# Performance work log

Measured on AMD Instinct MI355X. Metric: run time of the kernel, lower is better.

## Reference

```python
import jax, jax.numpy as jnp
import numpy as np

N_NODES = 50000
N_EDGES = 600000
N_GRAPHS = 64
D_FEAT = 128
DIM_H = 128
N_HOPS = 3
OUT_DIM = 10


def setup_inputs() -> dict:
    key = jax.random.key(0)
    ks = jax.random.split(key, 16)
    x = jax.random.normal(ks[0], (N_NODES, D_FEAT), dtype=jnp.float32)
    edge_index = jax.random.randint(ks[1], (2, N_EDGES), 0, N_NODES, dtype=jnp.int64)
    batch = jnp.sort(jax.random.randint(ks[2], (N_NODES,), 0, N_GRAPHS, dtype=jnp.int64))
    def glorot(k, shape):
        fan = shape[0] + shape[1]
        return jax.random.uniform(k, shape, jnp.float32, -1.0, 1.0) * np.sqrt(6.0 / fan)
    # GCNConv weights stored as [in, out]; Linear weights stored as [in, out]
    W1 = glorot(ks[3], (D_FEAT, DIM_H)); b1 = jnp.zeros((DIM_H,), jnp.float32)
    W2 = glorot(ks[4], (DIM_H, DIM_H)); b2 = jnp.zeros((DIM_H,), jnp.float32)
    W3 = glorot(ks[5], (DIM_H, DIM_H)); b3 = jnp.zeros((DIM_H,), jnp.float32)
    H3 = DIM_H * N_HOPS
    lin1_W = glorot(ks[6], (H3, H3)); lin1_b = jnp.zeros((H3,), jnp.float32)
    lin2_W = glorot(ks[7], (H3, OUT_DIM)); lin2_b = jnp.zeros((OUT_DIM,), jnp.float32)
    return {"x": x, "W1": W1, "b1": b1, "W2": W2, "b2": b2, "W3": W3, "b3": b3,
            "lin1_W": lin1_W, "lin1_b": lin1_b, "lin2_W": lin2_W, "lin2_b": lin2_b,
            "edge_index": edge_index, "batch": batch}


def gcn_conv(x, W, b, src, dst, n_nodes):
    # PyG GCNConv (add_self_loops=True, normalize=True):
    #   deg[i] = in-degree at target + 1 (self loop); norm = d^-1/2[src] * d^-1/2[dst]
    deg = jnp.zeros((n_nodes,), x.dtype).at[dst].add(1.0) + 1.0
    dinv = jax.lax.rsqrt(deg)
    xw = x @ W  # [N, H] transform before propagate
    coef = (dinv[src] * dinv[dst])[:, None]
    agg = jnp.zeros_like(xw).at[dst].add(xw[src] * coef)
    agg = agg + xw * (dinv * dinv)[:, None]  # self-loop messages
    return agg + b


def global_mean_pool(h, batch, n_graphs):
    sums = jax.ops.segment_sum(h, batch, num_segments=n_graphs)
    cnt = jax.ops.segment_sum(jnp.ones((h.shape[0],), h.dtype), batch, num_segments=n_graphs)
    return sums / jnp.maximum(cnt, 1.0)[:, None]


def reference(x, W1, b1, W2, b2, W3, b3, lin1_W, lin1_b, lin2_W, lin2_b, edge_index, batch):
    src, dst = edge_index[0], edge_index[1]
    n = x.shape[0]
    h1 = gcn_conv(x, W1, b1, src, dst, n)
    h2 = gcn_conv(h1, W2, b2, src, dst, n)
    h3 = gcn_conv(h2, W3, b3, src, dst, n)
    pooled = jnp.concatenate([global_mean_pool(h, batch, N_GRAPHS) for h in (h1, h2, h3)], axis=1)
    h = jax.nn.relu(pooled @ lin1_W + lin1_b)
    # dropout is identity in eval mode
    h = h @ lin2_W + lin2_b
    return (h, jax.nn.log_softmax(h, axis=1))
```

## Files before the change

kernel.cpp:

```cpp
#include <hip/hip_runtime.h>
#include <hip/hip_fp16.h>
#include <math.h>

#define N_NODES 50000
#define N_EDGES 600000
#define N_GRAPHS 64
#define DFEAT 128
#define H3 384
#define OUTD 10
#define SCAN_BLOCKS 196
#define POOL_CHUNKS 16
#define APAD 136

typedef _Float16 f16x8 __attribute__((ext_vector_type(8)));
typedef float f32x4 __attribute__((ext_vector_type(4)));
typedef float f32x2 __attribute__((ext_vector_type(2)));

__global__ __launch_bounds__(256) void k_deg(const int* __restrict__ ei, int* __restrict__ deg,
                                             int* __restrict__ rank) {
    int e = blockIdx.x * 256 + threadIdx.x;
    if (e >= N_EDGES) return;
    int dst = ei[N_EDGES + e];
    rank[e] = atomicAdd(&deg[dst], 1);
}

__global__ __launch_bounds__(256) void k_part(const int* __restrict__ deg, int* __restrict__ part) {
    __shared__ int red[256];
    int tid = threadIdx.x;
    int i = blockIdx.x * 256 + tid;
    red[tid] = (i < N_NODES) ? deg[i] : 0;
    __syncthreads();
    for (int s = 128; s > 0; s >>= 1) {
        if (tid < s) red[tid] += red[tid + s];
        __syncthreads();
    }
    if (tid == 0) part[blockIdx.x] = red[0];
}

__global__ __launch_bounds__(256) void k_scanpart(const int* __restrict__ part, int* __restrict__ base) {
    __shared__ int buf[256];
    int tid = threadIdx.x;
    int v = (tid < SCAN_BLOCKS) ? part[tid] : 0;
    buf[tid] = v;
    __syncthreads();
    for (int d = 1; d < 256; d <<= 1) {
        int t = (tid >= d) ? buf[tid - d] : 0;
        __syncthreads();
        buf[tid] += t;
        __syncthreads();
    }
    if (tid < SCAN_BLOCKS) base[tid] = buf[tid] - v;
}

__global__ __launch_bounds__(256) void k_offsets(const int* __restrict__ deg, const int* __restrict__ base,
                                                 int* __restrict__ offs, float* __restrict__ dinv) {
    __shared__ int buf[256];
    int tid = threadIdx.x;
    int i = blockIdx.x * 256 + tid;
    int v = (i < N_NODES) ? deg[i] : 0;
    buf[tid] = v;
    __syncthreads();
    for (int d = 1; d < 256; d <<= 1) {
        int t = (tid >= d) ? buf[tid - d] : 0;
        __syncthreads();
        buf[tid] += t;
        __syncthreads();
    }
    if (i < N_NODES) {
        int excl = base[blockIdx.x] + buf[tid] - v;
        offs[i] = excl;
        dinv[i] = rsqrtf((float)v + 1.0f);
        if (i == N_NODES - 1) offs[N_NODES] = base[blockIdx.x] + buf[tid];
    }
}

__global__ __launch_bounds__(256) void k_fill(const int* __restrict__ ei, const int* __restrict__ offs,
                                              const int* __restrict__ rank, const float* __restrict__ dinv,
                                              unsigned int* __restrict__ epack) {
    int e = blockIdx.x * 256 + threadIdx.x;
    if (e >= N_EDGES) return;
    int s = ei[e];
    int t = ei[N_EDGES + e];
    unsigned short dh = __half_as_ushort(__float2half(dinv[s]));
    epack[offs[t] + rank[e]] = (unsigned int)s | ((unsigned int)dh << 16);
}

__global__ __launch_bounds__(256) void k_prep(const float* __restrict__ W1, const float* __restrict__ W2,
                                              const float* __restrict__ W3, _Float16* __restrict__ Wt,
                                              float* __restrict__ pooled) {
    int b = blockIdx.x;
    if (b < 192) {
        int idx = b * 256 + threadIdx.x;
        int l = idx >> 14, r = idx & 16383;
        const float* W = (l == 0) ? W1 : (l == 1) ? W2 : W3;
        int k = r >> 7, n = r & 127;
        Wt[l * 16384 + n * 128 + k] = (_Float16)W[k * 128 + n];
    } else {
        int idx = (b - 192) * 256 + threadIdx.x;
        if (idx < N_GRAPHS * H3) pooled[idx] = 0.0f;
    }
}

template <bool A_FP16>
__global__ __launch_bounds__(256) void gemm_mfma(const void* __restrict__ Aptr, const _Float16* __restrict__ Wt,
                                                 unsigned char* __restrict__ T, int M) {
    __shared__ _Float16 As[64 * APAD];
    __shared__ _Float16 Ws[128 * APAD];
    int tid = threadIdx.x;
    int base = blockIdx.x * 64;
    for (int c = tid; c < 2048; c += 256) {
        int n = c >> 4, c8 = (c & 15) << 3;
        *(f16x8*)&Ws[n * APAD + c8] = *(const f16x8*)&Wt[n * 128 + c8];
    }
    for (int c = tid; c < 1024; c += 256) {
        int r = c >> 4, c8 = (c & 15) << 3;
        int gr = base + r; if (gr >= M) gr = M - 1;
        if (A_FP16) {
            const _Float16* A = (const _Float16*)Aptr;
            *(f16x8*)&As[r * APAD + c8] = *(const f16x8*)&A[(size_t)gr * 128 + c8];
        } else {
            const float* A = (const float*)Aptr;
            const float* src = A + (size_t)gr * 128 + c8;
            float4 v0 = *(const float4*)(src);
            float4 v1 = *(const float4*)(src + 4);
            f16x8 h;
            h[0] = (_Float16)v0.x; h[1] = (_Float16)v0.y; h[2] = (_Float16)v0.z; h[3] = (_Float16)v0.w;
            h[4] = (_Float16)v1.x; h[5] = (_Float16)v1.y; h[6] = (_Float16)v1.z; h[7] = (_Float16)v1.w;
            *(f16x8*)&As[r * APAD + c8] = h;
        }
    }
    __syncthreads();
    int wave = tid >> 6, lane = tid & 63;
    int m = lane & 15, quad = lane >> 4;
    f32x4 acc[8];
#pragma unroll
    for (int ct = 0; ct < 8; ++ct) acc[ct] = (f32x4){0.f, 0.f, 0.f, 0.f};
#pragma unroll
    for (int kc = 0; kc < 4; ++kc) {
        f16x8 a = *(const f16x8*)&As[(wave * 16 + m) * APAD + kc * 32 + quad * 8];
#pragma unroll
        for (int ct = 0; ct < 8; ++ct) {
            f16x8 b = *(const f16x8*)&Ws[(ct * 16 + m) * APAD + kc * 32 + quad * 8];
            acc[ct] = __builtin_amdgcn_mfma_f32_16x16x32_f16(b, a, acc[ct], 0, 0, 0);
        }
    }
    int node = base + wave * 16 + m;
    if (node < M) {
#pragma unroll
        for (int ct = 0; ct < 8; ++ct) {
            int col = ct * 16 + quad * 4;
            int p = __builtin_amdgcn_cvt_pk_fp8_f32(acc[ct][0], acc[ct][1], 0, false);
            p     = __builtin_amdgcn_cvt_pk_fp8_f32(acc[ct][2], acc[ct][3], p, true);
            *(int*)(T + (size_t)node * 128 + col) = p;
        }
    }
}

__global__ __launch_bounds__(128) void gather_agg(const unsigned int* __restrict__ T32,
                                                  const unsigned int* __restrict__ epack,
                                                  const int* __restrict__ offs,
                                                  const float* __restrict__ dinv, const float* __restrict__ bias,
                                                  __half2* __restrict__ H2) {
    int node = blockIdx.x * 2 + (threadIdx.x >> 6);
    int lane = threadIdx.x & 63;
    int half = lane >> 5, l32 = lane & 31;
    if (node >= N_NODES) return;
    float di = dinv[node];
    float a0 = 0.f, a1 = 0.f, a2 = 0.f, a3 = 0.f;
    int lo = offs[node], hi = offs[node + 1];
    int e = lo + half;
    for (; e + 7 <= hi; e += 8) {
        unsigned p0 = epack[e + 0], p1 = epack[e + 2], p2 = epack[e + 4], p3 = epack[e + 6];
        int s0 = p0 & 0xffff, s1 = p1 & 0xffff, s2 = p2 & 0xffff, s3 = p3 & 0xffff;
        float c0 = __half2float(__ushort_as_half((unsigned short)(p0 >> 16)));
        float c1 = __half2float(__ushort_as_half((unsigned short)(p1 >> 16)));
        float c2 = __half2float(__ushort_as_half((unsigned short)(p2 >> 16)));
        float c3 = __half2float(__ushort_as_half((unsigned short)(p3 >> 16)));
        unsigned u0 = T32[(size_t)s0 * 32 + l32];
        unsigned u1 = T32[(size_t)s1 * 32 + l32];
        unsigned u2 = T32[(size_t)s2 * 32 + l32];
        unsigned u3 = T32[(size_t)s3 * 32 + l32];
        f32x2 lo0 = __builtin_amdgcn_cvt_pk_f32_fp8(u0, false), hi0 = __builtin_amdgcn_cvt_pk_f32_fp8(u0, true);
        f32x2 lo1 = __builtin_amdgcn_cvt_pk_f32_fp8(u1, false), hi1 = __builtin_amdgcn_cvt_pk_f32_fp8(u1, true);
        f32x2 lo2 = __builtin_amdgcn_cvt_pk_f32_fp8(u2, false), hi2 = __builtin_amdgcn_cvt_pk_f32_fp8(u2, true);
        f32x2 lo3 = __builtin_amdgcn_cvt_pk_f32_fp8(u3, false), hi3 = __builtin_amdgcn_cvt_pk_f32_fp8(u3, true);
        a0 += lo0.x * c0; a1 += lo0.y * c0; a2 += hi0.x * c0; a3 += hi0.y * c0;
        a0 += lo1.x * c1; a1 += lo1.y * c1; a2 += hi1.x * c1; a3 += hi1.y * c1;
        a0 += lo2.x * c2; a1 += lo2.y * c2; a2 += hi2.x * c2; a3 += hi2.y * c2;
        a0 += lo3.x * c3; a1 += lo3.y * c3; a2 += hi3.x * c3; a3 += hi3.y * c3;
    }
    for (; e < hi; e += 2) {
        unsigned p = epack[e];
        int s = p & 0xffff;
        float c = __half2float(__ushort_as_half((unsigned short)(p >> 16)));
        unsigned u = T32[(size_t)s * 32 + l32];
        f32x2 tl = __builtin_amdgcn_cvt_pk_f32_fp8(u, false), th = __builtin_amdgcn_cvt_pk_f32_fp8(u, true);
        a0 += tl.x * c; a1 += tl.y * c; a2 += th.x * c; a3 += th.y * c;
    }
    a0 += __shfl_xor(a0, 32, 64);
    a1 += __shfl_xor(a1, 32, 64);
    a2 += __shfl_xor(a2, 32, 64);
    a3 += __shfl_xor(a3, 32, 64);
    if (half == 0) {
        unsigned su = T32[(size_t)node * 32 + l32];
        f32x2 sl = __builtin_amdgcn_cvt_pk_f32_fp8(su, false), sh = __builtin_amdgcn_cvt_pk_f32_fp8(su, true);
        float4 b4 = *(const float4*)(bias + l32 * 4);
        float dd = di * di;
        float r0 = di * a0 + sl.x * dd + b4.x;
        float r1 = di * a1 + sl.y * dd + b4.y;
        float r2 = di * a2 + sh.x * dd + b4.z;
        float r3 = di * a3 + sh.y * dd + b4.w;
        H2[(size_t)node * 64 + l32 * 2]     = __floats2half2_rn(r0, r1);
        H2[(size_t)node * 64 + l32 * 2 + 1] = __floats2half2_rn(r2, r3);
    }
}

__global__ __launch_bounds__(256) void pool_kernel(const __half2* __restrict__ H2, const int* __restrict__ batch,
                                                   float* __restrict__ pooled, int colOff) {
    __shared__ int bounds[2];
    __shared__ float2 red[256];
    int g = blockIdx.x >> 4;
    int chunk = blockIdx.x & (POOL_CHUNKS - 1);
    int tid = threadIdx.x;
    int d2 = tid & 63, sub = tid >> 6;
    if (tid < 2) {
        int target = g + tid;
        int lo = 0, hi = N_NODES;
        while (lo < hi) {
            int mid = (lo + hi) >> 1;
            if (batch[mid] < target) lo = mid + 1; else hi = mid;
        }
        bounds[tid] = lo;
    }
    __syncthreads();
    int lo = bounds[0], hi = bounds[1];
    int n = hi - lo;
    int per = (n + POOL_CHUNKS - 1) / POOL_CHUNKS;
    int s = lo + chunk * per;
    int e = s + per; if (e > hi) e = hi;
    float ax = 0.0f, ay = 0.0f;
    for (int r = s + sub; r < e; r += 4) {
        float2 v = __half22float2(H2[(size_t)r * 64 + d2]);
        ax += v.x; ay += v.y;
    }
    red[tid] = make_float2(ax, ay);
    __syncthreads();
    if (sub == 0 && s < e) {
        float2 v0 = red[d2], v1 = red[64 + d2], v2 = red[128 + d2], v3 = red[192 + d2];
        float vx = v0.x + v1.x + v2.x + v3.x;
        float vy = v0.y + v1.y + v2.y + v3.y;
        atomicAdd(&pooled[g * H3 + colOff + d2 * 2],     vx);
        atomicAdd(&pooled[g * H3 + colOff + d2 * 2 + 1], vy);
    }
}

__global__ __launch_bounds__(384) void mlp_kernel(const float* __restrict__ pooled,
                                                  const int* __restrict__ batch,
                                                  const float* __restrict__ l1W, const float* __restrict__ l1b,
                                                  const float* __restrict__ l2W, const float* __restrict__ l2b,
                                                  float* __restrict__ out) {
    __shared__ float p[H3];
    __shared__ float hid[H3];
    __shared__ float o10[OUTD];
    __shared__ int bnd[2];
    int g = blockIdx.x, tid = threadIdx.x;
    if (tid < 2) {
        int target = g + tid;
        int lo = 0, hi = N_NODES;
        while (lo < hi) {
            int mid = (lo + hi) >> 1;
            if (batch[mid] < target) lo = mid + 1; else hi = mid;
        }
        bnd[tid] = lo;
    }
    __syncthreads();
    float inv = 1.0f / fmaxf((float)(bnd[1] - bnd[0]), 1.0f);
    p[tid] = pooled[g * H3 + tid] * inv;
    __syncthreads();
    float acc = l1b[tid];
    for (int k = 0; k < H3; ++k) acc += p[k] * l1W[k * H3 + tid];
    hid[tid] = fmaxf(acc, 0.0f);
    __syncthreads();
    if (tid < OUTD) {
        float o = l2b[tid];
        for (int k = 0; k < H3; ++k) o += hid[k] * l2W[k * OUTD + tid];
        o10[tid] = o;
        out[g * OUTD + tid] = o;
    }
    __syncthreads();
    if (tid == 0) {
        float m = o10[0];
        for (int j = 1; j < OUTD; ++j) m = fmaxf(m, o10[j]);
        float s = 0.0f;
        for (int j = 0; j < OUTD; ++j) s += expf(o10[j] - m);
        float lse = m + logf(s);
        for (int j = 0; j < OUTD; ++j) out[N_GRAPHS * OUTD + g * OUTD + j] = o10[j] - lse;
    }
}

extern "C" void kernel_launch(void* const* d_in, const int* in_sizes, int n_in,
                              void* d_out, int out_size, void* d_ws, size_t ws_size,
                              hipStream_t stream) {
    const float* x      = (const float*)d_in[0];
    const float* W1     = (const float*)d_in[1];
    const float* b1     = (const float*)d_in[2];
    const float* W2     = (const float*)d_in[3];
    const float* b2     = (const float*)d_in[4];
    const float* W3     = (const float*)d_in[5];
    const float* b3     = (const float*)d_in[6];
    const float* lin1_W = (const float*)d_in[7];
    const float* lin1_b = (const float*)d_in[8];
    const float* lin2_W = (const float*)d_in[9];
    const float* lin2_b = (const float*)d_in[10];
    const int* edge_index = (const int*)d_in[11];
    const int* batch      = (const int*)d_in[12];

    char* ws = (char*)d_ws;
    auto alloc = [&](size_t bytes) -> void* {
        void* p = (void*)ws;
        ws += (bytes + 255) & ~(size_t)255;
        return p;
    };
    int*   deg    = (int*)  alloc((size_t)N_NODES * 4);
    int*   part   = (int*)  alloc((size_t)SCAN_BLOCKS * 4);
    int*   pbase  = (int*)  alloc((size_t)SCAN_BLOCKS * 4);
    int*   offs   = (int*)  alloc((size_t)(N_NODES + 1) * 4);
    int*   rank   = (int*)  alloc((size_t)N_EDGES * 4);
    float* dinv   = (float*)alloc((size_t)N_NODES * 4);
    unsigned int* epack = (unsigned int*)alloc((size_t)N_EDGES * 4);
    unsigned char* T = (unsigned char*)alloc((size_t)N_NODES * 128);
    __half* H     = (__half*)alloc((size_t)N_NODES * 128 * 2);
    _Float16* Wt  = (_Float16*)alloc((size_t)3 * 128 * 128 * 2);
    float* pooled = (float*)alloc((size_t)N_GRAPHS * H3 * 4);

    hipMemsetAsync(deg, 0, (size_t)N_NODES * 4, stream);
    k_deg<<<(N_EDGES + 255) / 256, 256, 0, stream>>>(edge_index, deg, rank);
    k_part<<<SCAN_BLOCKS, 256, 0, stream>>>(deg, part);
    k_scanpart<<<1, 256, 0, stream>>>(part, pbase);
    k_offsets<<<SCAN_BLOCKS, 256, 0, stream>>>(deg, pbase, offs, dinv);
    k_fill<<<(N_EDGES + 255) / 256, 256, 0, stream>>>(edge_index, offs, rank, dinv, epack);
    k_prep<<<288, 256, 0, stream>>>(W1, W2, W3, Wt, pooled);

    const float* bs[3] = {b1, b2, b3};
    for (int l = 0; l < 3; ++l) {
        if (l == 0)
            gemm_mfma<false><<<(N_NODES + 63) / 64, 256, 0, stream>>>(x, Wt, T, N_NODES);
        else
            gemm_mfma<true><<<(N_NODES + 63) / 64, 256, 0, stream>>>(H, Wt + (size_t)l * 16384, T, N_NODES);
        gather_agg<<<(N_NODES + 1) / 2, 128, 0, stream>>>((const unsigned int*)T, epack, offs, dinv, bs[l], (__half2*)H);
        pool_kernel<<<N_GRAPHS * POOL_CHUNKS, 256, 0, stream>>>((const __half2*)H, batch, pooled, l * 128);
    }
    mlp_kernel<<<N_GRAPHS, 384, 0, stream>>>(pooled, batch, lin1_W, lin1_b, lin2_W, lin2_b, (float*)d_out);
}
```

Before: 309.0 us.

## Use one half-wave per node in gather and pool all layers in one launch

The gather kernel now gives each node its own 32-lane group that walks every edge with an 8-way unrolled load batch, replacing the old scheme where two half-waves split a node's edges and combined them with a cross-lane shuffle. Each layer writes to its own H buffer, so the three pool launches become one kernel that loops over the layers after all convolutions finish. This is meant to raise memory-level parallelism and remove launches and shuffles, at the cost of extra workspace and possible load imbalance on high-degree nodes. The gather grid uses N_NODES/4 with no bounds check, which is only safe because N_NODES divides evenly by 4.

```diff
diff --git a/kernel.cpp b/kernel.cpp
--- a/kernel.cpp
+++ b/kernel.cpp
@@ -161,62 +161,73 @@
                                                   const int* __restrict__ offs,
                                                   const float* __restrict__ dinv, const float* __restrict__ bias,
                                                   __half2* __restrict__ H2) {
-    int node = blockIdx.x * 2 + (threadIdx.x >> 6);
-    int lane = threadIdx.x & 63;
-    int half = lane >> 5, l32 = lane & 31;
-    if (node >= N_NODES) return;
+    int h = threadIdx.x >> 5;
+    int l32 = threadIdx.x & 31;
+    int node = blockIdx.x * 4 + h;
     float di = dinv[node];
     float a0 = 0.f, a1 = 0.f, a2 = 0.f, a3 = 0.f;
     int lo = offs[node], hi = offs[node + 1];
-    int e = lo + half;
-    for (; e + 7 <= hi; e += 8) {
-        unsigned p0 = epack[e + 0], p1 = epack[e + 2], p2 = epack[e + 4], p3 = epack[e + 6];
-        int s0 = p0 & 0xffff, s1 = p1 & 0xffff, s2 = p2 & 0xffff, s3 = p3 & 0xffff;
+    int e = lo;
+    for (; e + 8 <= hi; e += 8) {
+        unsigned p0 = epack[e + 0], p1 = epack[e + 1], p2 = epack[e + 2], p3 = epack[e + 3];
+        unsigned p4 = epack[e + 4], p5 = epack[e + 5], p6 = epack[e + 6], p7 = epack[e + 7];
+        unsigned u0 = T32[(size_t)(p0 & 0xffff) * 32 + l32];
+        unsigned u1 = T32[(size_t)(p1 & 0xffff) * 32 + l32];
+        unsigned u2 = T32[(size_t)(p2 & 0xffff) * 32 + l32];
+        unsigned u3 = T32[(size_t)(p3 & 0xffff) * 32 + l32];
+        unsigned u4 = T32[(size_t)(p4 & 0xffff) * 32 + l32];
+        unsigned u5 = T32[(size_t)(p5 & 0xffff) * 32 + l32];
+        unsigned u6 = T32[(size_t)(p6 & 0xffff) * 32 + l32];
+        unsigned u7 = T32[(size_t)(p7 & 0xffff) * 32 + l32];
         float c0 = __half2float(__ushort_as_half((unsigned short)(p0 >> 16)));
         float c1 = __half2float(__ushort_as_half((unsigned short)(p1 >> 16)));
         float c2 = __half2float(__ushort_as_half((unsigned short)(p2 >> 16)));
         float c3 = __half2float(__ushort_as_half((unsigned short)(p3 >> 16)));
-        unsigned u0 = T32[(size_t)s0 * 32 + l32];
-        unsigned u1 = T32[(size_t)s1 * 32 + l32];
-        unsigned u2 = T32[(size_t)s2 * 32 + l32];
-        unsigned u3 = T32[(size_t)s3 * 32 + l32];
+        float c4 = __half2float(__ushort_as_half((unsigned short)(p4 >> 16)));
+        float c5 = __half2float(__ushort_as_half((unsigned short)(p5 >> 16)));
+        float c6 = __half2float(__ushort_as_half((unsigned short)(p6 >> 16)));
+        float c7 = __half2float(__ushort_as_half((unsigned short)(p7 >> 16)));
         f32x2 lo0 = __builtin_amdgcn_cvt_pk_f32_fp8(u0, false), hi0 = __builtin_amdgcn_cvt_pk_f32_fp8(u0, true);
         f32x2 lo1 = __builtin_amdgcn_cvt_pk_f32_fp8(u1, false), hi1 = __builtin_amdgcn_cvt_pk_f32_fp8(u1, true);
         f32x2 lo2 = __builtin_amdgcn_cvt_pk_f32_fp8(u2, false), hi2 = __builtin_amdgcn_cvt_pk_f32_fp8(u2, true);
         f32x2 lo3 = __builtin_amdgcn_cvt_pk_f32_fp8(u3, false), hi3 = __builtin_amdgcn_cvt_pk_f32_fp8(u3, true);
+        f32x2 lo4 = __builtin_amdgcn_cvt_pk_f32_fp8(u4, false), hi4 = __builtin_amdgcn_cvt_pk_f32_fp8(u4, true);
+        f32x2 lo5 = __builtin_amdgcn_cvt_pk_f32_fp8(u5, false), hi5 = __builtin_amdgcn_cvt_pk_f32_fp8(u5, true);
+        f32x2 lo6 = __builtin_amdgcn_cvt_pk_f32_fp8(u6, false), hi6 = __builtin_amdgcn_cvt_pk_f32_fp8(u6, true);
+        f32x2 lo7 = __builtin_amdgcn_cvt_pk_f32_fp8(u7, false), hi7 = __builtin_amdgcn_cvt_pk_f32_fp8(u7, true);
         a0 += lo0.x * c0; a1 += lo0.y * c0; a2 += hi0.x * c0; a3 += hi0.y * c0;
         a0 += lo1.x * c1; a1 += lo1.y * c1; a2 += hi1.x * c1; a3 += hi1.y * c1;
         a0 += lo2.x * c2; a1 += lo2.y * c2; a2 += hi2.x * c2; a3 += hi2.y * c2;
         a0 += lo3.x * c3; a1 += lo3.y * c3; a2 += hi3.x * c3; a3 += hi3.y * c3;
-    }
-    for (; e < hi; e += 2) {
+        a0 += lo4.x * c4; a1 += lo4.y * c4; a2 += hi4.x * c4; a3 += hi4.y * c4;
+        a0 += lo5.x * c5; a1 += lo5.y * c5; a2 += hi5.x * c5; a3 += hi5.y * c5;
+        a0 += lo6.x * c6; a1 += lo6.y * c6; a2 += hi6.x * c6; a3 += hi6.y * c6;
+        a0 += lo7.x * c7; a1 += lo7.y * c7; a2 += hi7.x * c7; a3 += hi7.y * c7;
+    }
+    for (; e < hi; ++e) {
         unsigned p = epack[e];
-        int s = p & 0xffff;
         float c = __half2float(__ushort_as_half((unsigned short)(p >> 16)));
-        unsigned u = T32[(size_t)s * 32 + l32];
+        unsigned u = T32[(size_t)(p & 0xffff) * 32 + l32];
         f32x2 tl = __builtin_amdgcn_cvt_pk_f32_fp8(u, false), th = __builtin_amdgcn_cvt_pk_f32_fp8(u, true);
         a0 += tl.x * c; a1 += tl.y * c; a2 += th.x * c; a3 += th.y * c;
     }
-    a0 += __shfl_xor(a0, 32, 64);
-    a1 += __shfl_xor(a1, 32, 64);
-    a2 += __shfl_xor(a2, 32, 64);
-    a3 += __shfl_xor(a3, 32, 64);
-    if (half == 0) {
-        unsigned su = T32[(size_t)node * 32 + l32];
-        f32x2 sl = __builtin_amdgcn_cvt_pk_f32_fp8(su, false), sh = __builtin_amdgcn_cvt_pk_f32_fp8(su, true);
-        float4 b4 = *(const float4*)(bias + l32 * 4);
-        float dd = di * di;
-        float r0 = di * a0 + sl.x * dd + b4.x;
-        float r1 = di * a1 + sl.y * dd + b4.y;
-        float r2 = di * a2 + sh.x * dd + b4.z;
-        float r3 = di * a3 + sh.y * dd + b4.w;
-        H2[(size_t)node * 64 + l32 * 2]     = __floats2half2_rn(r0, r1);
-        H2[(size_t)node * 64 + l32 * 2 + 1] = __floats2half2_rn(r2, r3);
-    }
-}
-
-__global__ __launch_bounds__(256) void pool_kernel(const __half2* __restrict__ H2, const int* __restrict__ batch,
-                                                   float* __restrict__ pooled, int colOff) {
+    unsigned su = T32[(size_t)node * 32 + l32];
+    f32x2 sl = __builtin_amdgcn_cvt_pk_f32_fp8(su, false), sh = __builtin_amdgcn_cvt_pk_f32_fp8(su, true);
+    float4 b4 = *(const float4*)(bias + l32 * 4);
+    float dd = di * di;
+    float r0 = di * a0 + sl.x * dd + b4.x;
+    float r1 = di * a1 + sl.y * dd + b4.y;
+    float r2 = di * a2 + sh.x * dd + b4.z;
+    float r3 = di * a3 + sh.y * dd + b4.w;
+    H2[(size_t)node * 64 + l32 * 2]     = __floats2half2_rn(r0, r1);
+    H2[(size_t)node * 64 + l32 * 2 + 1] = __floats2half2_rn(r2, r3);
+}
+
+__global__ __launch_bounds__(256) void pool_kernel(const __half2* __restrict__ H0,
+                                                   const __half2* __restrict__ H1,
+                                                   const __half2* __restrict__ H2buf,
+                                                   const int* __restrict__ batch,
+                                                   float* __restrict__ pooled) {
     __shared__ int bounds[2];
     __shared__ float2 red[256];
     int g = blockIdx.x >> 4;
@@ -238,19 +249,22 @@
     int per = (n + POOL_CHUNKS - 1) / POOL_CHUNKS;
     int s = lo + chunk * per;
     int e = s + per; if (e > hi) e = hi;
-    float ax = 0.0f, ay = 0.0f;
-    for (int r = s + sub; r < e; r += 4) {
-        float2 v = __half22float2(H2[(size_t)r * 64 + d2]);
-        ax += v.x; ay += v.y;
-    }
-    red[tid] = make_float2(ax, ay);
-    __syncthreads();
-    if (sub == 0 && s < e) {
-        float2 v0 = red[d2], v1 = red[64 + d2], v2 = red[128 + d2], v3 = red[192 + d2];
-        float vx = v0.x + v1.x + v2.x + v3.x;
-        float vy = v0.y + v1.y + v2.y + v3.y;
-        atomicAdd(&pooled[g * H3 + colOff + d2 * 2],     vx);
-        atomicAdd(&pooled[g * H3 + colOff + d2 * 2 + 1], vy);
+    const __half2* Hs[3] = {H0, H1, H2buf};
+    for (int l = 0; l < 3; ++l) {
+        const __half2* H = Hs[l];
+        float ax = 0.0f, ay = 0.0f;
+        for (int r = s + sub; r < e; r += 4) {
+            float2 v = __half22float2(H[(size_t)r * 64 + d2]);
+            ax += v.x; ay += v.y;
+        }
+        red[tid] = make_float2(ax, ay);
+        __syncthreads();
+        if (sub == 0 && s < e) {
+            float2 v0 = red[d2], v1 = red[64 + d2], v2 = red[128 + d2], v3 = red[192 + d2];
+            atomicAdd(&pooled[g * H3 + l * 128 + d2 * 2],     v0.x + v1.x + v2.x + v3.x);
+            atomicAdd(&pooled[g * H3 + l * 128 + d2 * 2 + 1], v0.y + v1.y + v2.y + v3.y);
+        }
+        __syncthreads();
     }
 }
 
@@ -329,7 +343,8 @@
     float* dinv   = (float*)alloc((size_t)N_NODES * 4);
     unsigned int* epack = (unsigned int*)alloc((size_t)N_EDGES * 4);
     unsigned char* T = (unsigned char*)alloc((size_t)N_NODES * 128);
-    __half* H     = (__half*)alloc((size_t)N_NODES * 128 * 2);
+    __half* Hbuf[3];
+    for (int l = 0; l < 3; ++l) Hbuf[l] = (__half*)alloc((size_t)N_NODES * 128 * 2);
     _Float16* Wt  = (_Float16*)alloc((size_t)3 * 128 * 128 * 2);
     float* pooled = (float*)alloc((size_t)N_GRAPHS * H3 * 4);
 
@@ -346,9 +361,10 @@
         if (l == 0)
             gemm_mfma<false><<<(N_NODES + 63) / 64, 256, 0, stream>>>(x, Wt, T, N_NODES);
         else
-            gemm_mfma<true><<<(N_NODES + 63) / 64, 256, 0, stream>>>(H, Wt + (size_t)l * 16384, T, N_NODES);
-        gather_agg<<<(N_NODES + 1) / 2, 128, 0, stream>>>((const unsigned int*)T, epack, offs, dinv, bs[l], (__half2*)H);
-        pool_kernel<<<N_GRAPHS * POOL_CHUNKS, 256, 0, stream>>>((const __half2*)H, batch, pooled, l * 128);
-    }
+            gemm_mfma<true><<<(N_NODES + 63) / 64, 256, 0, stream>>>(Hbuf[l - 1], Wt + (size_t)l * 16384, T, N_NODES);
+        gather_agg<<<N_NODES / 4, 128, 0, stream>>>((const unsigned int*)T, epack, offs, dinv, bs[l], (__half2*)Hbuf[l]);
+    }
+    pool_kernel<<<N_GRAPHS * POOL_CHUNKS, 256, 0, stream>>>((const __half2*)Hbuf[0], (const __half2*)Hbuf[1],
+                                                            (const __half2*)Hbuf[2], batch, pooled);
     mlp_kernel<<<N_GRAPHS, 384, 0, stream>>>(pooled, batch, lin1_W, lin1_b, lin2_W, lin2_b, (float*)d_out);
 }
```

New measurement: 296.7 us. 4.0% less time.
